# Kernel tuning notes

Measured on AMD Instinct MI355X. Metric: run time of the kernel, lower is better.

The kernel has to match this reference:

```python
import jax, jax.numpy as jnp
import numpy as np

EPS = 1e-6
SLIDING_WINDOW = 512
ROPE_BASE = 10000.0  # rope_local_base_freq for sliding_attention layers


def _rms_norm(x, w=None):
    # Gemma-style RMSNorm computed in fp32 then cast back
    xf = x.astype(jnp.float32)
    out = xf * jax.lax.rsqrt(jnp.mean(xf * xf, axis=-1, keepdims=True) + EPS)
    if w is not None:
        out = out * w.astype(jnp.float32)
    return out.astype(x.dtype)


def _rotate_half(x):
    x1, x2 = jnp.split(x, 2, axis=-1)
    return jnp.concatenate((-x2, x1), axis=-1)


def setup_inputs() -> dict:
    key = jax.random.key(0)
    ks = jax.random.split(key, 6)
    B, S, H, NH, NKV, D = 1, 4096, 2048, 8, 2, 256
    hidden_states = jax.random.normal(ks[0], (B, S, H), dtype=jnp.float32)
    w_q = jax.random.normal(ks[1], (H, NH * D), dtype=jnp.float32) * 0.02
    w_k = jax.random.normal(ks[2], (H, NKV * D), dtype=jnp.float32) * 0.02
    w_v = jax.random.normal(ks[3], (H, NKV * D), dtype=jnp.float32) * 0.02
    w_o = jax.random.normal(ks[4], (NH * D, H), dtype=jnp.float32) * 0.02
    q_norm_w = jnp.ones((D,), dtype=jnp.float32)
    k_norm_w = jnp.ones((D,), dtype=jnp.float32)
    # RoPE tables (local base freq, sliding layer)
    inv_freq = 1.0 / (ROPE_BASE ** (jnp.arange(0, D, 2, dtype=jnp.float32) / D))
    pos = jnp.arange(S, dtype=jnp.float32)
    freqs = pos[:, None] * inv_freq[None, :]          # [S, D/2]
    emb = jnp.concatenate((freqs, freqs), axis=-1)    # [S, D]
    cos = jnp.broadcast_to(jnp.cos(emb)[None], (B, S, D)).astype(jnp.float32)
    sin = jnp.broadcast_to(jnp.sin(emb)[None], (B, S, D)).astype(jnp.float32)
    return {"hidden_states": hidden_states, "w_q": w_q, "w_k": w_k, "w_v": w_v,
            "w_o": w_o, "q_norm_w": q_norm_w, "k_norm_w": k_norm_w,
            "cos": cos, "sin": sin}


def reference(hidden_states, w_q, w_k, w_v, w_o, q_norm_w, k_norm_w, cos, sin):
    B, S, _ = hidden_states.shape
    D = cos.shape[-1]
    NH = w_q.shape[1] // D
    NKV = w_k.shape[1] // D
    G = NH // NKV

    # projections -> [B, S, heads, D], per-head RMSNorm (Gemma3n-style)
    q = _rms_norm((hidden_states @ w_q).reshape(B, S, NH, D), q_norm_w)
    k = _rms_norm((hidden_states @ w_k).reshape(B, S, NKV, D), k_norm_w)
    v = _rms_norm((hidden_states @ w_v).reshape(B, S, NKV, D))  # v_norm: no scale

    q = q.transpose(0, 2, 1, 3)  # [B, NH, S, D]
    k = k.transpose(0, 2, 1, 3)  # [B, NKV, S, D]
    v = v.transpose(0, 2, 1, 3)

    # RoPE, cos/sin unsqueezed over the head dim
    c = cos[:, None, :, :]
    s = sin[:, None, :, :]
    q = q * c + _rotate_half(q) * s
    k = k * c + _rotate_half(k) * s

    # GQA: repeat KV heads
    k = jnp.repeat(k, G, axis=1)  # [B, NH, S, D]
    v = jnp.repeat(v, G, axis=1)

    # attention, scaling = 1.0 (q_norm replaces 1/sqrt(d) in this family)
    scores = jnp.einsum('bhqd,bhkd->bhqk', q, k)

    # causal + sliding-window mask
    i = jnp.arange(S)[:, None]
    j = jnp.arange(S)[None, :]
    mask = (j <= i) & ((i - j) < SLIDING_WINDOW)
    scores = jnp.where(mask[None, None], scores, jnp.finfo(scores.dtype).min)

    attn = jax.nn.softmax(scores.astype(jnp.float32), axis=-1).astype(q.dtype)
    out = jnp.einsum('bhqk,bhkd->bhqd', attn, v)
    out = out.transpose(0, 2, 1, 3).reshape(B, S, NH * D)
    return out @ w_o
```

## Files before the change

### kernel.cpp

```cpp
#include <hip/hip_runtime.h>
#include <hip/hip_bf16.h>

#define S_LEN 4096
#define HDIM  2048
#define NHQ   8
#define NKVH  2
#define DHEAD 256
#define WIN   512
#define NQKV  3072

typedef __hip_bfloat16 bf16_t;
using fragAB = __attribute__((ext_vector_type(8))) short;
using fragC  = __attribute__((ext_vector_type(4))) float;

typedef unsigned int u32;
typedef const __attribute__((address_space(1))) u32* gas_ptr;
typedef __attribute__((address_space(3))) u32* las_ptr;

__device__ __forceinline__ void async_copy16(const void* g, void* l) {
  __builtin_amdgcn_global_load_lds((gas_ptr)g, (las_ptr)l, 16, 0, 0);
}

#define NEG_BIG (-3.0e38f)

__device__ __forceinline__ void split2(float x, bf16_t& hi, bf16_t& lo) {
  bf16_t h = __float2bfloat16(x);
  hi = h;
  lo = __float2bfloat16(x - (float)h);
}

__global__ __launch_bounds__(256) void split_f32(
    const float* __restrict__ in, bf16_t* __restrict__ hi,
    bf16_t* __restrict__ lo, int n) {
  int i = (blockIdx.x * 256 + threadIdx.x) * 4;
  if (i >= n) return;
  float4 v = *(const float4*)(in + i);
  split2(v.x, hi[i + 0], lo[i + 0]);
  split2(v.y, hi[i + 1], lo[i + 1]);
  split2(v.z, hi[i + 2], lo[i + 2]);
  split2(v.w, hi[i + 3], lo[i + 3]);
}

__global__ __launch_bounds__(256) void transpose_cvt(
    const float* __restrict__ in, bf16_t* __restrict__ out, int R, int C) {
  __shared__ bf16_t tile[32][33];
  int c0 = blockIdx.x * 32, r0 = blockIdx.y * 32;
  int tx = threadIdx.x & 31, ty = threadIdx.x >> 5;
#pragma unroll
  for (int i = 0; i < 4; ++i)
    tile[ty + i * 8][tx] = __float2bfloat16(in[(size_t)(r0 + ty + i * 8) * C + c0 + tx]);
  __syncthreads();
#pragma unroll
  for (int i = 0; i < 4; ++i)
    out[(size_t)(c0 + ty + i * 8) * R + r0 + tx] = tile[tx][ty + i * 8];
}

__global__ __launch_bounds__(256) void transpose_split(
    const float* __restrict__ in, bf16_t* __restrict__ hiT,
    bf16_t* __restrict__ loT, int R, int C) {
  __shared__ bf16_t th[32][33];
  __shared__ bf16_t tl[32][33];
  int c0 = blockIdx.x * 32, r0 = blockIdx.y * 32;
  int tx = threadIdx.x & 31, ty = threadIdx.x >> 5;
#pragma unroll
  for (int i = 0; i < 4; ++i) {
    float x = in[(size_t)(r0 + ty + i * 8) * C + c0 + tx];
    bf16_t h, l; split2(x, h, l);
    th[ty + i * 8][tx] = h;
    tl[ty + i * 8][tx] = l;
  }
  __syncthreads();
#pragma unroll
  for (int i = 0; i < 4; ++i) {
    hiT[(size_t)(c0 + ty + i * 8) * R + r0 + tx] = th[tx][ty + i * 8];
    loT[(size_t)(c0 + ty + i * 8) * R + r0 + tx] = tl[tx][ty + i * 8];
  }
}

template <typename OutT>
__global__ __launch_bounds__(256) void gemm_bt(
    const bf16_t* __restrict__ A, const bf16_t* __restrict__ Bt,
    OutT* __restrict__ C, int M, int N, int K) {
  __shared__ __align__(16) bf16_t As[128 * 32];
  __shared__ __align__(16) bf16_t Bs[128 * 32];
  const int t = threadIdx.x;
  const int wave = t >> 6, lane = t & 63;
  const int quad = lane >> 4, l16 = lane & 15;
  const int m0 = blockIdx.y * 128, n0 = blockIdx.x * 128;
  const int wm = (wave >> 1) * 64, wn = (wave & 1) * 64;

  fragC zero4 = {0.f, 0.f, 0.f, 0.f};
  fragC acc[4][4];
#pragma unroll
  for (int i = 0; i < 4; ++i)
#pragma unroll
    for (int j = 0; j < 4; ++j) acc[i][j] = zero4;

  int rowS[2], colS[2];
#pragma unroll
  for (int i = 0; i < 2; ++i) {
    int e = (wave * 2048 + i * 1024 + lane * 16) >> 1;
    rowS[i] = e >> 5;
    colS[i] = e & 31;
  }

  for (int k0 = 0; k0 < K; k0 += 32) {
#pragma unroll
    for (int i = 0; i < 2; ++i) {
      async_copy16(A + (size_t)(m0 + rowS[i]) * K + k0 + colS[i],
                   (char*)As + wave * 2048 + i * 1024);
      async_copy16(Bt + (size_t)(n0 + rowS[i]) * K + k0 + colS[i],
                   (char*)Bs + wave * 2048 + i * 1024);
    }
    __syncthreads();
    fragAB af[4], bfr[4];
#pragma unroll
    for (int i = 0; i < 4; ++i) {
      af[i]  = *(const fragAB*)((const char*)As + (wm + i * 16 + l16) * 64 + quad * 16);
      bfr[i] = *(const fragAB*)((const char*)Bs + (wn + i * 16 + l16) * 64 + quad * 16);
    }
#pragma unroll
    for (int i = 0; i < 4; ++i)
#pragma unroll
      for (int j = 0; j < 4; ++j)
        acc[i][j] = __builtin_amdgcn_mfma_f32_16x16x32_bf16(af[i], bfr[j], acc[i][j], 0, 0, 0);
    __syncthreads();
  }

#pragma unroll
  for (int i = 0; i < 4; ++i)
#pragma unroll
    for (int j = 0; j < 4; ++j)
#pragma unroll
      for (int r = 0; r < 4; ++r) {
        int row = m0 + wm + i * 16 + quad * 4 + r;
        int col = n0 + wn + j * 16 + l16;
        float v = acc[i][j][r];
        if constexpr (sizeof(OutT) == 2)
          C[(size_t)row * N + col] = (OutT)__float2bfloat16(v);
        else
          C[(size_t)row * N + col] = (OutT)v;
      }
}

#define OFF_AH 0
#define OFF_AL 16384
#define OFF_BH 32768
#define OFF_BL 45056
#define BUFSZ  57344

#define VMCNT_(n) asm volatile("s_waitcnt vmcnt(" #n ")" ::: "memory")
#define VMCNT(n) VMCNT_(n)
#define BARRIER()                     \
  {                                   \
    asm volatile("" ::: "memory");    \
    __builtin_amdgcn_s_barrier();     \
    asm volatile("" ::: "memory");    \
  }

#define MFMA_(a, b, c) __builtin_amdgcn_mfma_f32_16x16x32_bf16(a, b, c, 0, 0, 0)

#define LOADB()                                                   \
  _Pragma("unroll")                                               \
  for (int j = 0; j < 3; ++j) {                                   \
    const char* bp_ = bufc + (wn + j * 16 + l16) * 64 + rdq;      \
    bh[j] = *(const fragAB*)(bp_ + OFF_BH);                       \
    bl[j] = *(const fragAB*)(bp_ + OFF_BL);                       \
  }

#define PHASEP(p)                                                        \
  {                                                                      \
    const char* a0p_ = bufc + (wm + (2 * (p)) * 16 + l16) * 64 + rdq;    \
    const char* a1p_ = bufc + (wm + (2 * (p) + 1) * 16 + l16) * 64 + rdq;\
    fragAB ah0 = *(const fragAB*)(a0p_ + OFF_AH);                        \
    fragAB al0 = *(const fragAB*)(a0p_ + OFF_AL);                        \
    fragAB ah1 = *(const fragAB*)(a1p_ + OFF_AH);                        \
    fragAB al1 = *(const fragAB*)(a1p_ + OFF_AL);                        \
    __builtin_amdgcn_s_setprio(1);                                       \
    _Pragma("unroll")                                                    \
    for (int j = 0; j < 3; ++j) {                                        \
      acc[2 * (p)][j]     = MFMA_(al0, bh[j], acc[2 * (p)][j]);          \
      acc[2 * (p)][j]     = MFMA_(ah0, bl[j], acc[2 * (p)][j]);          \
      acc[2 * (p)][j]     = MFMA_(ah0, bh[j], acc[2 * (p)][j]);          \
      acc[2 * (p) + 1][j] = MFMA_(al1, bh[j], acc[2 * (p) + 1][j]);      \
      acc[2 * (p) + 1][j] = MFMA_(ah1, bl[j], acc[2 * (p) + 1][j]);      \
      acc[2 * (p) + 1][j] = MFMA_(ah1, bh[j], acc[2 * (p) + 1][j]);      \
    }                                                                    \
    __builtin_amdgcn_s_setprio(0);                                       \
  }

__global__ __launch_bounds__(512, 2) void gemm_split2(
    const bf16_t* __restrict__ Ah, const bf16_t* __restrict__ Al,
    const bf16_t* __restrict__ Bh, const bf16_t* __restrict__ Bl,
    float* __restrict__ C, int M, int N, int K) {
  __shared__ __align__(16) char lds[2 * BUFSZ];
  const int t = threadIdx.x;
  const int wave = t >> 6, lane = t & 63;
  const int quad = lane >> 4, l16 = lane & 15;
  const int m0 = blockIdx.y * 256, n0 = blockIdx.x * 192;
  const int wm = (wave >> 2) * 128, wn = (wave & 3) * 48;
  const int rdq = (quad ^ ((l16 >> 1) & 3)) * 16;

  const size_t laneOff =
      (size_t)(lane >> 2) * K * 2 + 16 * ((lane & 3) ^ ((lane >> 3) & 3));

  const char* gsrc[7];
  int ldsOff[7];
#pragma unroll
  for (int pos = 0; pos < 3; ++pos) {
    int c = wave + 8 * pos;
    if (c < 12) {
      gsrc[pos]   = (const char*)Bh + (size_t)(n0 + 16 * c) * K * 2 + laneOff;
      ldsOff[pos] = OFF_BH + c * 1024;
    } else {
      gsrc[pos]   = (const char*)Bl + (size_t)(n0 + 16 * (c - 12)) * K * 2 + laneOff;
      ldsOff[pos] = OFF_BL + (c - 12) * 1024;
    }
  }
#pragma unroll
  for (int p = 0; p < 4; ++p) {
    int sub = wave & 3;
    int R0 = ((sub >> 1) & 1) * 128 + 32 * p + (sub & 1) * 16;
    const char* base = (const char*)(wave < 4 ? Ah : Al);
    gsrc[3 + p]   = base + (size_t)(m0 + R0) * K * 2 + laneOff;
    ldsOff[3 + p] = (wave < 4 ? OFF_AH : OFF_AL) + R0 * 64;
  }

  fragC zero4 = {0.f, 0.f, 0.f, 0.f};
  fragC acc[8][3];
#pragma unroll
  for (int i = 0; i < 8; ++i)
#pragma unroll
    for (int j = 0; j < 3; ++j) acc[i][j] = zero4;

  char* ldsc = (char*)lds;
#pragma unroll
  for (int ps = 0; ps < 7; ++ps) async_copy16(gsrc[ps], ldsc + ldsOff[ps]);
#pragma unroll
  for (int ps = 0; ps < 7; ++ps) gsrc[ps] += 64;

  fragAB bh[3], bl[3];
  int cur = 0;
  const int NS = K / 32;
  for (int it = 0; it < NS - 1; ++it) {
    const char* bufc = ldsc + cur * BUFSZ;
    char* nb = ldsc + (cur ^ 1) * BUFSZ;
#pragma unroll
    for (int ps = 0; ps < 7; ++ps) async_copy16(gsrc[ps], nb + ldsOff[ps]);
#pragma unroll
    for (int ps = 0; ps < 7; ++ps) gsrc[ps] += 64;
    VMCNT(10); BARRIER();
    LOADB();
    PHASEP(0);
    VMCNT(9); BARRIER();
    PHASEP(1);
    VMCNT(8); BARRIER();
    PHASEP(2);
    VMCNT(7); BARRIER();
    PHASEP(3);
    BARRIER();
    cur ^= 1;
  }
  {
    const char* bufc = ldsc + cur * BUFSZ;
    VMCNT(3); BARRIER();
    LOADB();
    PHASEP(0);
    VMCNT(2); BARRIER();
    PHASEP(1);
    VMCNT(1); BARRIER();
    PHASEP(2);
    VMCNT(0); BARRIER();
    PHASEP(3);
  }

#pragma unroll
  for (int i = 0; i < 8; ++i)
#pragma unroll
    for (int j = 0; j < 3; ++j)
#pragma unroll
      for (int r = 0; r < 4; ++r) {
        int row = m0 + wm + i * 16 + quad * 4 + r;
        int col = n0 + wn + j * 16 + l16;
        C[(size_t)row * N + col] = acc[i][j][r];
      }
}

__global__ __launch_bounds__(256) void rmsnorm_rope_split(
    const float* __restrict__ proj, const float* __restrict__ w,
    const float* __restrict__ cosb, const float* __restrict__ sinb,
    bf16_t* __restrict__ qhi, bf16_t* __restrict__ qlo,
    int inStride, int inOff, int outStride) {
  int s = blockIdx.x, h = blockIdx.y, d = threadIdx.x;
  float x = proj[(size_t)s * inStride + inOff + h * DHEAD + d];
  float ss = x * x;
  ss += __shfl_xor(ss, 1);  ss += __shfl_xor(ss, 2);  ss += __shfl_xor(ss, 4);
  ss += __shfl_xor(ss, 8);  ss += __shfl_xor(ss, 16); ss += __shfl_xor(ss, 32);
  __shared__ float part[4];
  __shared__ float xs[DHEAD];
  if ((threadIdx.x & 63) == 0) part[threadIdx.x >> 6] = ss;
  __syncthreads();
  float tot = part[0] + part[1] + part[2] + part[3];
  float r = rsqrtf(tot * (1.0f / DHEAD) + 1e-6f);
  float xn = x * r * w[d];
  xs[d] = xn;
  __syncthreads();
  float other = xs[(d + 128) & 255];
  float rot = (d < 128) ? -other : other;
  float y = xn * cosb[(size_t)s * DHEAD + d] + rot * sinb[(size_t)s * DHEAD + d];
  bf16_t h2, l2; split2(y, h2, l2);
  size_t oidx = (size_t)s * outStride + h * DHEAD + d;
  qhi[oidx] = h2;
  qlo[oidx] = l2;
}

__global__ __launch_bounds__(256) void rmsnorm_vT(
    const float* __restrict__ proj, bf16_t* __restrict__ vt,
    int inStride, int inOff) {
  int s = blockIdx.x, h = blockIdx.y, d = threadIdx.x;
  float x = proj[(size_t)s * inStride + inOff + h * DHEAD + d];
  float ss = x * x;
  ss += __shfl_xor(ss, 1);  ss += __shfl_xor(ss, 2);  ss += __shfl_xor(ss, 4);
  ss += __shfl_xor(ss, 8);  ss += __shfl_xor(ss, 16); ss += __shfl_xor(ss, 32);
  __shared__ float part[4];
  if ((threadIdx.x & 63) == 0) part[threadIdx.x >> 6] = ss;
  __syncthreads();
  float tot = part[0] + part[1] + part[2] + part[3];
  float r = rsqrtf(tot * (1.0f / DHEAD) + 1e-6f);
  vt[((size_t)h * DHEAD + d) * S_LEN + s] = __float2bfloat16(x * r);
}

__global__ __launch_bounds__(256) void attn_split(
    const bf16_t* __restrict__ Qhi, const bf16_t* __restrict__ Qlo,
    const bf16_t* __restrict__ Khi, const bf16_t* __restrict__ Klo,
    const bf16_t* __restrict__ Vt, bf16_t* __restrict__ Aout) {
  const int h = blockIdx.y;
  const int qb = blockIdx.x * 64;
  const int wave = threadIdx.x >> 6, lane = threadIdx.x & 63;
  const int quad = lane >> 4, l16 = lane & 15;
  const int qw = qb + wave * 16;
  const int kv = h >> 2;
  const bf16_t* Qh_ = Qhi + h * DHEAD;
  const bf16_t* Ql_ = Qlo + h * DHEAD;
  const bf16_t* Kh_ = Khi + kv * DHEAD;
  const bf16_t* Kl_ = Klo + kv * DHEAD;
  const bf16_t* Vh_ = Vt + (size_t)kv * DHEAD * S_LEN;

  __shared__ __align__(16) bf16_t KshH[32 * 256];
  __shared__ __align__(16) bf16_t KshL[32 * 256];
  __shared__ __align__(16) bf16_t Vsh[256 * 32];
  __shared__ __align__(16) bf16_t Plds[4][16 * 32];

  fragAB qfh[8], qfl[8];
#pragma unroll
  for (int c = 0; c < 8; ++c) {
    size_t off = (size_t)(qw + l16) * (NHQ * DHEAD) + c * 32 + quad * 8;
    qfh[c] = *(const fragAB*)(Qh_ + off);
    qfl[c] = *(const fragAB*)(Ql_ + off);
  }

  int kRow[4], kCol[4], vRow[4], vCol[4];
#pragma unroll
  for (int i = 0; i < 4; ++i) {
    int ci = (i * 4 + wave) * 64 + lane;
    int r = ci >> 5, sc = ci & 31;
    kRow[i] = r;
    kCol[i] = (sc ^ r) * 8;
    int rv = ci >> 2, scv = ci & 3;
    vRow[i] = rv;
    vCol[i] = (scv ^ (rv & 3)) * 8;
  }

  fragC zero4 = {0.f, 0.f, 0.f, 0.f};
  fragC o_acc[16];
#pragma unroll
  for (int c = 0; c < 16; ++c) o_acc[c] = zero4;
  float m_run[4] = {NEG_BIG, NEG_BIG, NEG_BIG, NEG_BIG};
  float l_run[4] = {0.f, 0.f, 0.f, 0.f};
  const float LOG2E = 1.4426950408889634f;

  int k_lo = qb - (WIN - 1);
  if (k_lo < 0) k_lo = 0;
  k_lo &= ~31;

  for (int kb = k_lo; kb < qb + 64; kb += 32) {
#pragma unroll
    for (int i = 0; i < 4; ++i) {
      size_t dst = (size_t)(i * 4 + wave) * 1024;
      size_t koff = (size_t)(kb + kRow[i]) * (NKVH * DHEAD) + kCol[i];
      async_copy16(Kh_ + koff, (char*)KshH + dst);
      async_copy16(Kl_ + koff, (char*)KshL + dst);
      async_copy16(Vh_ + (size_t)vRow[i] * S_LEN + kb + vCol[i], (char*)Vsh + dst);
    }
    __syncthreads();

    fragC s0 = zero4, s1 = zero4;
#pragma unroll
    for (int c = 0; c < 8; ++c) {
      int j = c * 4 + quad;
      int off0 = (l16 * 32 + (j ^ l16)) * 16;
      int off1 = ((16 + l16) * 32 + (j ^ (16 + l16))) * 16;
      fragAB kh0 = *(const fragAB*)((const char*)KshH + off0);
      fragAB kl0 = *(const fragAB*)((const char*)KshL + off0);
      fragAB kh1 = *(const fragAB*)((const char*)KshH + off1);
      fragAB kl1 = *(const fragAB*)((const char*)KshL + off1);
      s0 = __builtin_amdgcn_mfma_f32_16x16x32_bf16(qfl[c], kh0, s0, 0, 0, 0);
      s0 = __builtin_amdgcn_mfma_f32_16x16x32_bf16(qfh[c], kl0, s0, 0, 0, 0);
      s0 = __builtin_amdgcn_mfma_f32_16x16x32_bf16(qfh[c], kh0, s0, 0, 0, 0);
      s1 = __builtin_amdgcn_mfma_f32_16x16x32_bf16(qfl[c], kh1, s1, 0, 0, 0);
      s1 = __builtin_amdgcn_mfma_f32_16x16x32_bf16(qfh[c], kl1, s1, 0, 0, 0);
      s1 = __builtin_amdgcn_mfma_f32_16x16x32_bf16(qfh[c], kh1, s1, 0, 0, 0);
    }

    float p0[4], p1[4], alpha[4];
#pragma unroll
    for (int r = 0; r < 4; ++r) {
      int qi = qw + quad * 4 + r;
      int k0i = kb + l16;
      int k1i = k0i + 16;
      bool v0 = (k0i <= qi) && (qi - k0i < WIN);
      bool v1 = (k1i <= qi) && (qi - k1i < WIN);
      float sv0 = v0 ? s0[r] : NEG_BIG;
      float sv1 = v1 ? s1[r] : NEG_BIG;
      float mx = fmaxf(sv0, sv1);
      mx = fmaxf(mx, __shfl_xor(mx, 1));
      mx = fmaxf(mx, __shfl_xor(mx, 2));
      mx = fmaxf(mx, __shfl_xor(mx, 4));
      mx = fmaxf(mx, __shfl_xor(mx, 8));
      float mn = fmaxf(m_run[r], mx);
      float a  = exp2f(fmaxf(m_run[r] - mn, -80.f) * LOG2E);
      float e0 = v0 ? exp2f(fmaxf(s0[r] - mn, -80.f) * LOG2E) : 0.f;
      float e1 = v1 ? exp2f(fmaxf(s1[r] - mn, -80.f) * LOG2E) : 0.f;
      float rs = e0 + e1;
      rs += __shfl_xor(rs, 1);
      rs += __shfl_xor(rs, 2);
      rs += __shfl_xor(rs, 4);
      rs += __shfl_xor(rs, 8);
      l_run[r] = l_run[r] * a + rs;
      m_run[r] = mn;
      alpha[r] = a; p0[r] = e0; p1[r] = e1;
    }
#pragma unroll
    for (int c = 0; c < 16; ++c)
#pragma unroll
      for (int r = 0; r < 4; ++r) o_acc[c][r] *= alpha[r];

    bf16_t* Pw = Plds[wave];
#pragma unroll
    for (int r = 0; r < 4; ++r) {
      Pw[(quad * 4 + r) * 32 + l16]      = __float2bfloat16(p0[r]);
      Pw[(quad * 4 + r) * 32 + 16 + l16] = __float2bfloat16(p1[r]);
    }
    fragAB pf = *(const fragAB*)((const char*)Pw + l16 * 64 + quad * 16);

#pragma unroll
    for (int c = 0; c < 16; ++c) {
      int d = c * 16 + l16;
      int offv = (d * 4 + (quad ^ (d & 3))) * 16;
      fragAB vf = *(const fragAB*)((const char*)Vsh + offv);
      o_acc[c] = __builtin_amdgcn_mfma_f32_16x16x32_bf16(pf, vf, o_acc[c], 0, 0, 0);
    }
    __syncthreads();
  }

  float inv_l[4];
#pragma unroll
  for (int r = 0; r < 4; ++r) inv_l[r] = 1.0f / l_run[r];
#pragma unroll
  for (int c = 0; c < 16; ++c)
#pragma unroll
    for (int r = 0; r < 4; ++r) {
      int row = qw + quad * 4 + r;
      int col = h * DHEAD + c * 16 + l16;
      Aout[(size_t)row * (NHQ * DHEAD) + col] = __float2bfloat16(o_acc[c][r] * inv_l[r]);
    }
}

extern "C" void kernel_launch(void* const* d_in, const int* in_sizes, int n_in,
                              void* d_out, int out_size, void* d_ws, size_t ws_size,
                              hipStream_t stream) {
  const float* hid  = (const float*)d_in[0];
  const float* w_q  = (const float*)d_in[1];
  const float* w_k  = (const float*)d_in[2];
  const float* w_v  = (const float*)d_in[3];
  const float* w_o  = (const float*)d_in[4];
  const float* qnw  = (const float*)d_in[5];
  const float* knw  = (const float*)d_in[6];
  const float* cosb = (const float*)d_in[7];
  const float* sinb = (const float*)d_in[8];
  float* outp = (float*)d_out;

  const size_t M1 = 1048576;
  bf16_t* w = (bf16_t*)d_ws;
  bf16_t* hidh  = w;
  bf16_t* qh    = w;
  bf16_t* hidl  = w + 8 * M1;
  bf16_t* ql    = w + 8 * M1;
  bf16_t* wTh   = w + 16 * M1;
  bf16_t* kh    = w + 16 * M1;
  bf16_t* kl    = w + 18 * M1;
  bf16_t* vt    = w + 20 * M1;
  bf16_t* wTl   = w + 22 * M1;
  bf16_t* woT   = w + 22 * M1;
  float*  projqkv = (float*)(w + 28 * M1);
  bf16_t* aout  = w + 28 * M1;

  split_f32<<<(S_LEN * HDIM) / 1024, 256, 0, stream>>>(hid, hidh, hidl, S_LEN * HDIM);
  transpose_split<<<dim3((NHQ * DHEAD) / 32, HDIM / 32), 256, 0, stream>>>(
      w_q, wTh, wTl, HDIM, NHQ * DHEAD);
  transpose_split<<<dim3((NKVH * DHEAD) / 32, HDIM / 32), 256, 0, stream>>>(
      w_k, wTh + (size_t)(NHQ * DHEAD) * HDIM, wTl + (size_t)(NHQ * DHEAD) * HDIM,
      HDIM, NKVH * DHEAD);
  transpose_split<<<dim3((NKVH * DHEAD) / 32, HDIM / 32), 256, 0, stream>>>(
      w_v, wTh + (size_t)(NHQ * DHEAD + NKVH * DHEAD) * HDIM,
      wTl + (size_t)(NHQ * DHEAD + NKVH * DHEAD) * HDIM, HDIM, NKVH * DHEAD);

  gemm_split2<<<dim3(NQKV / 192, S_LEN / 256), 512, 0, stream>>>(
      hidh, hidl, wTh, wTl, projqkv, S_LEN, NQKV, HDIM);

  rmsnorm_rope_split<<<dim3(S_LEN, NHQ), 256, 0, stream>>>(
      projqkv, qnw, cosb, sinb, qh, ql, NQKV, 0, NHQ * DHEAD);
  rmsnorm_rope_split<<<dim3(S_LEN, NKVH), 256, 0, stream>>>(
      projqkv, knw, cosb, sinb, kh, kl, NQKV, NHQ * DHEAD, NKVH * DHEAD);
  rmsnorm_vT<<<dim3(S_LEN, NKVH), 256, 0, stream>>>(
      projqkv, vt, NQKV, NHQ * DHEAD + NKVH * DHEAD);

  transpose_cvt<<<dim3(HDIM / 32, (NHQ * DHEAD) / 32), 256, 0, stream>>>(w_o, woT, NHQ * DHEAD, HDIM);

  attn_split<<<dim3(S_LEN / 64, NHQ), 256, 0, stream>>>(qh, ql, kh, kl, vt, aout);

  gemm_bt<float><<<dim3(HDIM / 128, S_LEN / 128), 256, 0, stream>>>(aout, woT, outp, S_LEN, HDIM, NHQ * DHEAD);
}
```

Measured before the change: 473.6 us.

## Software-pipeline LDS fragment loads in split GEMM and add pipelined output GEMM

The split-bf16 QKV GEMM now loads the A fragments for the next phase into a second register set before issuing the current phase's MFMAs. The MFMAs are also reordered so that consecutive instructions do not depend on the same accumulator, and the vmcnt waits are adjusted to match. The simple 128x128 output-projection GEMM is replaced by a 256x128-tile, 512-thread kernel. That kernel uses double-buffered async global-to-LDS loads, XOR-swizzled LDS, K-step 64 and the same phased pipeline. This is meant to hide LDS and global latency behind MFMA, at the cost of more registers and tighter wait-count bookkeeping.

```diff
diff --git a/kernel.cpp b/kernel.cpp
--- a/kernel.cpp
+++ b/kernel.cpp
@@ -77,78 +77,6 @@
   }
 }
 
-template <typename OutT>
-__global__ __launch_bounds__(256) void gemm_bt(
-    const bf16_t* __restrict__ A, const bf16_t* __restrict__ Bt,
-    OutT* __restrict__ C, int M, int N, int K) {
-  __shared__ __align__(16) bf16_t As[128 * 32];
-  __shared__ __align__(16) bf16_t Bs[128 * 32];
-  const int t = threadIdx.x;
-  const int wave = t >> 6, lane = t & 63;
-  const int quad = lane >> 4, l16 = lane & 15;
-  const int m0 = blockIdx.y * 128, n0 = blockIdx.x * 128;
-  const int wm = (wave >> 1) * 64, wn = (wave & 1) * 64;
-
-  fragC zero4 = {0.f, 0.f, 0.f, 0.f};
-  fragC acc[4][4];
-#pragma unroll
-  for (int i = 0; i < 4; ++i)
-#pragma unroll
-    for (int j = 0; j < 4; ++j) acc[i][j] = zero4;
-
-  int rowS[2], colS[2];
-#pragma unroll
-  for (int i = 0; i < 2; ++i) {
-    int e = (wave * 2048 + i * 1024 + lane * 16) >> 1;
-    rowS[i] = e >> 5;
-    colS[i] = e & 31;
-  }
-
-  for (int k0 = 0; k0 < K; k0 += 32) {
-#pragma unroll
-    for (int i = 0; i < 2; ++i) {
-      async_copy16(A + (size_t)(m0 + rowS[i]) * K + k0 + colS[i],
-                   (char*)As + wave * 2048 + i * 1024);
-      async_copy16(Bt + (size_t)(n0 + rowS[i]) * K + k0 + colS[i],
-                   (char*)Bs + wave * 2048 + i * 1024);
-    }
-    __syncthreads();
-    fragAB af[4], bfr[4];
-#pragma unroll
-    for (int i = 0; i < 4; ++i) {
-      af[i]  = *(const fragAB*)((const char*)As + (wm + i * 16 + l16) * 64 + quad * 16);
-      bfr[i] = *(const fragAB*)((const char*)Bs + (wn + i * 16 + l16) * 64 + quad * 16);
-    }
-#pragma unroll
-    for (int i = 0; i < 4; ++i)
-#pragma unroll
-      for (int j = 0; j < 4; ++j)
-        acc[i][j] = __builtin_amdgcn_mfma_f32_16x16x32_bf16(af[i], bfr[j], acc[i][j], 0, 0, 0);
-    __syncthreads();
-  }
-
-#pragma unroll
-  for (int i = 0; i < 4; ++i)
-#pragma unroll
-    for (int j = 0; j < 4; ++j)
-#pragma unroll
-      for (int r = 0; r < 4; ++r) {
-        int row = m0 + wm + i * 16 + quad * 4 + r;
-        int col = n0 + wn + j * 16 + l16;
-        float v = acc[i][j][r];
-        if constexpr (sizeof(OutT) == 2)
-          C[(size_t)row * N + col] = (OutT)__float2bfloat16(v);
-        else
-          C[(size_t)row * N + col] = (OutT)v;
-      }
-}
-
-#define OFF_AH 0
-#define OFF_AL 16384
-#define OFF_BH 32768
-#define OFF_BL 45056
-#define BUFSZ  57344
-
 #define VMCNT_(n) asm volatile("s_waitcnt vmcnt(" #n ")" ::: "memory")
 #define VMCNT(n) VMCNT_(n)
 #define BARRIER()                     \
@@ -160,6 +88,12 @@
 
 #define MFMA_(a, b, c) __builtin_amdgcn_mfma_f32_16x16x32_bf16(a, b, c, 0, 0, 0)
 
+#define OFF_AH 0
+#define OFF_AL 16384
+#define OFF_BH 32768
+#define OFF_BL 45056
+#define BUFSZ  57344
+
 #define LOADB()                                                   \
   _Pragma("unroll")                                               \
   for (int j = 0; j < 3; ++j) {                                   \
@@ -168,26 +102,39 @@
     bl[j] = *(const fragAB*)(bp_ + OFF_BL);                       \
   }
 
-#define PHASEP(p)                                                        \
-  {                                                                      \
-    const char* a0p_ = bufc + (wm + (2 * (p)) * 16 + l16) * 64 + rdq;    \
-    const char* a1p_ = bufc + (wm + (2 * (p) + 1) * 16 + l16) * 64 + rdq;\
-    fragAB ah0 = *(const fragAB*)(a0p_ + OFF_AH);                        \
-    fragAB al0 = *(const fragAB*)(a0p_ + OFF_AL);                        \
-    fragAB ah1 = *(const fragAB*)(a1p_ + OFF_AH);                        \
-    fragAB al1 = *(const fragAB*)(a1p_ + OFF_AL);                        \
-    __builtin_amdgcn_s_setprio(1);                                       \
-    _Pragma("unroll")                                                    \
-    for (int j = 0; j < 3; ++j) {                                        \
-      acc[2 * (p)][j]     = MFMA_(al0, bh[j], acc[2 * (p)][j]);          \
-      acc[2 * (p)][j]     = MFMA_(ah0, bl[j], acc[2 * (p)][j]);          \
-      acc[2 * (p)][j]     = MFMA_(ah0, bh[j], acc[2 * (p)][j]);          \
-      acc[2 * (p) + 1][j] = MFMA_(al1, bh[j], acc[2 * (p) + 1][j]);      \
-      acc[2 * (p) + 1][j] = MFMA_(ah1, bl[j], acc[2 * (p) + 1][j]);      \
-      acc[2 * (p) + 1][j] = MFMA_(ah1, bh[j], acc[2 * (p) + 1][j]);      \
-    }                                                                    \
-    __builtin_amdgcn_s_setprio(0);                                       \
-  }
+struct ARegs { fragAB ah0, al0, ah1, al1; };
+
+__device__ __forceinline__ void lda_split(ARegs& r, const char* bufc, int wm,
+                                          int p, int l16, int rdq) {
+  const char* a0 = bufc + (wm + (2 * p) * 16 + l16) * 64 + rdq;
+  const char* a1 = a0 + 16 * 64;
+  r.ah0 = *(const fragAB*)(a0 + OFF_AH);
+  r.al0 = *(const fragAB*)(a0 + OFF_AL);
+  r.ah1 = *(const fragAB*)(a1 + OFF_AH);
+  r.al1 = *(const fragAB*)(a1 + OFF_AL);
+}
+
+__device__ __forceinline__ void mfma_split(fragC (&acc)[8][3], const ARegs& r,
+                                           const fragAB (&bh)[3],
+                                           const fragAB (&bl)[3], int p) {
+  __builtin_amdgcn_s_setprio(1);
+#pragma unroll
+  for (int j = 0; j < 3; ++j) {
+    acc[2 * p][j]     = MFMA_(r.al0, bh[j], acc[2 * p][j]);
+    acc[2 * p + 1][j] = MFMA_(r.al1, bh[j], acc[2 * p + 1][j]);
+  }
+#pragma unroll
+  for (int j = 0; j < 3; ++j) {
+    acc[2 * p][j]     = MFMA_(r.ah0, bl[j], acc[2 * p][j]);
+    acc[2 * p + 1][j] = MFMA_(r.ah1, bl[j], acc[2 * p + 1][j]);
+  }
+#pragma unroll
+  for (int j = 0; j < 3; ++j) {
+    acc[2 * p][j]     = MFMA_(r.ah0, bh[j], acc[2 * p][j]);
+    acc[2 * p + 1][j] = MFMA_(r.ah1, bh[j], acc[2 * p + 1][j]);
+  }
+  __builtin_amdgcn_s_setprio(0);
+}
 
 __global__ __launch_bounds__(512, 2) void gemm_split2(
     const bf16_t* __restrict__ Ah, const bf16_t* __restrict__ Al,
@@ -240,6 +187,7 @@
   for (int ps = 0; ps < 7; ++ps) gsrc[ps] += 64;
 
   fragAB bh[3], bl[3];
+  ARegs r0, r1;
   int cur = 0;
   const int NS = K / 32;
   for (int it = 0; it < NS - 1; ++it) {
@@ -249,35 +197,179 @@
     for (int ps = 0; ps < 7; ++ps) async_copy16(gsrc[ps], nb + ldsOff[ps]);
 #pragma unroll
     for (int ps = 0; ps < 7; ++ps) gsrc[ps] += 64;
-    VMCNT(10); BARRIER();
+    VMCNT(9); BARRIER();
     LOADB();
-    PHASEP(0);
-    VMCNT(9); BARRIER();
-    PHASEP(1);
+    lda_split(r0, bufc, wm, 0, l16, rdq);
+    lda_split(r1, bufc, wm, 1, l16, rdq);
+    mfma_split(acc, r0, bh, bl, 0);
     VMCNT(8); BARRIER();
-    PHASEP(2);
+    lda_split(r0, bufc, wm, 2, l16, rdq);
+    mfma_split(acc, r1, bh, bl, 1);
     VMCNT(7); BARRIER();
-    PHASEP(3);
+    lda_split(r1, bufc, wm, 3, l16, rdq);
+    mfma_split(acc, r0, bh, bl, 2);
+    mfma_split(acc, r1, bh, bl, 3);
     BARRIER();
     cur ^= 1;
   }
   {
     const char* bufc = ldsc + cur * BUFSZ;
-    VMCNT(3); BARRIER();
+    VMCNT(2); BARRIER();
     LOADB();
-    PHASEP(0);
+    lda_split(r0, bufc, wm, 0, l16, rdq);
+    lda_split(r1, bufc, wm, 1, l16, rdq);
+    mfma_split(acc, r0, bh, bl, 0);
+    VMCNT(1); BARRIER();
+    lda_split(r0, bufc, wm, 2, l16, rdq);
+    mfma_split(acc, r1, bh, bl, 1);
+    VMCNT(0); BARRIER();
+    lda_split(r1, bufc, wm, 3, l16, rdq);
+    mfma_split(acc, r0, bh, bl, 2);
+    mfma_split(acc, r1, bh, bl, 3);
+  }
+
+#pragma unroll
+  for (int i = 0; i < 8; ++i)
+#pragma unroll
+    for (int j = 0; j < 3; ++j)
+#pragma unroll
+      for (int r = 0; r < 4; ++r) {
+        int row = m0 + wm + i * 16 + quad * 4 + r;
+        int col = n0 + wn + j * 16 + l16;
+        C[(size_t)row * N + col] = acc[i][j][r];
+      }
+}
+
+#define BT_OFF_A 0
+#define BT_OFF_B 32768
+#define BT_BUFSZ 49152
+
+struct ARegs2 { fragAB a[2][2]; };
+
+__device__ __forceinline__ void lda_bt(ARegs2& r, const char* bufc, int wm,
+                                       int p, int l16, int quad, int rx) {
+#pragma unroll
+  for (int u = 0; u < 2; ++u)
+#pragma unroll
+    for (int ks = 0; ks < 2; ++ks)
+      r.a[u][ks] = *(const fragAB*)(bufc + BT_OFF_A +
+                                    (wm + (2 * p + u) * 16 + l16) * 128 +
+                                    (((ks * 4 + quad) ^ rx) * 16));
+}
+
+__device__ __forceinline__ void mfma_bt(fragC (&acc)[8][2], const ARegs2& r,
+                                        const fragAB (&b)[2][2], int p) {
+  __builtin_amdgcn_s_setprio(1);
+#pragma unroll
+  for (int ks = 0; ks < 2; ++ks)
+#pragma unroll
+    for (int j = 0; j < 2; ++j) {
+      acc[2 * p][j]     = MFMA_(r.a[0][ks], b[j][ks], acc[2 * p][j]);
+      acc[2 * p + 1][j] = MFMA_(r.a[1][ks], b[j][ks], acc[2 * p + 1][j]);
+    }
+  __builtin_amdgcn_s_setprio(0);
+}
+
+__global__ __launch_bounds__(512, 2) void gemm_bt2(
+    const bf16_t* __restrict__ A, const bf16_t* __restrict__ Bt,
+    float* __restrict__ C, int M, int N, int K) {
+  __shared__ __align__(16) char lds[2 * BT_BUFSZ];
+  const int t = threadIdx.x;
+  const int wave = t >> 6, lane = t & 63;
+  const int quad = lane >> 4, l16 = lane & 15;
+  const int m0 = blockIdx.y * 256, n0 = blockIdx.x * 128;
+  const int wm = (wave >> 2) * 128, wn = (wave & 3) * 32;
+  const int rx = l16 & 7;
+
+  const size_t laneOff =
+      (size_t)(lane >> 3) * K * 2 + 16 * ((lane & 7) ^ ((lane >> 3) & 7));
+
+  const char* gsrc[6];
+  int ldsOff[6];
+#pragma unroll
+  for (int pos = 0; pos < 2; ++pos) {
+    int c = wave + 8 * pos;
+    gsrc[pos]   = (const char*)Bt + (size_t)(n0 + 8 * c) * K * 2 + laneOff;
+    ldsOff[pos] = BT_OFF_B + c * 1024;
+  }
+#pragma unroll
+  for (int p = 0; p < 4; ++p) {
+    int R0 = (wave >> 2) * 128 + 32 * p + (wave & 3) * 8;
+    gsrc[2 + p]   = (const char*)A + (size_t)(m0 + R0) * K * 2 + laneOff;
+    ldsOff[2 + p] = BT_OFF_A + R0 * 128;
+  }
+
+  fragC zero4 = {0.f, 0.f, 0.f, 0.f};
+  fragC acc[8][2];
+#pragma unroll
+  for (int i = 0; i < 8; ++i)
+#pragma unroll
+    for (int j = 0; j < 2; ++j) acc[i][j] = zero4;
+
+  char* ldsc = (char*)lds;
+#pragma unroll
+  for (int ps = 0; ps < 6; ++ps) async_copy16(gsrc[ps], ldsc + ldsOff[ps]);
+#pragma unroll
+  for (int ps = 0; ps < 6; ++ps) gsrc[ps] += 128;
+
+  fragAB bfr[2][2];
+  ARegs2 r0, r1;
+  int cur = 0;
+  const int NS = K / 64;
+  for (int it = 0; it < NS - 1; ++it) {
+    const char* bufc = ldsc + cur * BT_BUFSZ;
+    char* nb = ldsc + (cur ^ 1) * BT_BUFSZ;
+#pragma unroll
+    for (int ps = 0; ps < 6; ++ps) async_copy16(gsrc[ps], nb + ldsOff[ps]);
+#pragma unroll
+    for (int ps = 0; ps < 6; ++ps) gsrc[ps] += 128;
+    VMCNT(8); BARRIER();
+#pragma unroll
+    for (int j = 0; j < 2; ++j)
+#pragma unroll
+      for (int ks = 0; ks < 2; ++ks)
+        bfr[j][ks] = *(const fragAB*)(bufc + BT_OFF_B +
+                                      (wn + j * 16 + l16) * 128 +
+                                      (((ks * 4 + quad) ^ rx) * 16));
+    lda_bt(r0, bufc, wm, 0, l16, quad, rx);
+    lda_bt(r1, bufc, wm, 1, l16, quad, rx);
+    mfma_bt(acc, r0, bfr, 0);
+    VMCNT(7); BARRIER();
+    lda_bt(r0, bufc, wm, 2, l16, quad, rx);
+    mfma_bt(acc, r1, bfr, 1);
+    VMCNT(6); BARRIER();
+    lda_bt(r1, bufc, wm, 3, l16, quad, rx);
+    mfma_bt(acc, r0, bfr, 2);
+    mfma_bt(acc, r1, bfr, 3);
+    BARRIER();
+    cur ^= 1;
+  }
+  {
+    const char* bufc = ldsc + cur * BT_BUFSZ;
     VMCNT(2); BARRIER();
-    PHASEP(1);
+#pragma unroll
+    for (int j = 0; j < 2; ++j)
+#pragma unroll
+      for (int ks = 0; ks < 2; ++ks)
+        bfr[j][ks] = *(const fragAB*)(bufc + BT_OFF_B +
+                                      (wn + j * 16 + l16) * 128 +
+                                      (((ks * 4 + quad) ^ rx) * 16));
+    lda_bt(r0, bufc, wm, 0, l16, quad, rx);
+    lda_bt(r1, bufc, wm, 1, l16, quad, rx);
+    mfma_bt(acc, r0, bfr, 0);
     VMCNT(1); BARRIER();
-    PHASEP(2);
+    lda_bt(r0, bufc, wm, 2, l16, quad, rx);
+    mfma_bt(acc, r1, bfr, 1);
     VMCNT(0); BARRIER();
-    PHASEP(3);
+    lda_bt(r1, bufc, wm, 3, l16, quad, rx);
+    mfma_bt(acc, r0, bfr, 2);
+    mfma_bt(acc, r1, bfr, 3);
   }
 
 #pragma unroll
   for (int i = 0; i < 8; ++i)
 #pragma unroll
-    for (int j = 0; j < 3; ++j)
+    for (int j = 0; j < 2; ++j)
 #pragma unroll
       for (int r = 0; r < 4; ++r) {
         int row = m0 + wm + i * 16 + quad * 4 + r;
@@ -529,5 +621,6 @@
 
   attn_split<<<dim3(S_LEN / 64, NHQ), 256, 0, stream>>>(qh, ql, kh, kl, vt, aout);
 
-  gemm_bt<float><<<dim3(HDIM / 128, S_LEN / 128), 256, 0, stream>>>(aout, woT, outp, S_LEN, HDIM, NHQ * DHEAD);
-}
+  gemm_bt2<<<dim3(HDIM / 128, S_LEN / 256), 512, 0, stream>>>(
+      aout, woT, outp, S_LEN, HDIM, NHQ * DHEAD);
+}
```

After: 457.7 us. 3.4% less time.
